# Performance work log

Measured on AMD Instinct MI355X. Metric: run time of the kernel, lower is better.

## Reference

```python
import jax, jax.numpy as jnp
import numpy as np

WINDOW_SIZE = (8, 8, 8)
DIM = 256
NUM_HEADS = 8
NUM_WINDOWS = 16
BATCH = 128  # num_windows * B
N = int(np.prod(WINDOW_SIZE))  # 512


def _make_rpb_buffers(ws):
    space = len(ws)
    coords = [np.arange(-(w - 1), w, dtype=np.float32) for w in ws]
    rpb = np.stack(np.meshgrid(*coords, indexing='ij'))  # (space, 2w-1, ...)
    for i in range(space):
        rpb[i] = rpb[i] / (ws[i] - 1)
    rpb = np.moveaxis(rpb, 0, -1)[None]  # (1, ..., space)
    rpb = 8.0 * rpb
    rpb = np.sign(rpb) * np.log2(np.abs(rpb) + 1.0) / np.log2(8.0)
    grid = np.stack(np.meshgrid(*[np.arange(w) for w in ws], indexing='ij'))
    g = grid.reshape(space, -1).astype(np.int64)
    dists = g[:, :, None] - g[:, None, :]  # (space, N, N)
    for i in range(space):
        center = max(int(np.prod([2 * w - 1 for w in ws[i + 1:]])), 1)
        dists[i] = (dists[i] + ws[i] - 1) * center
    rpb_idx = dists.sum(0)  # (N, N)
    return rpb.astype(np.float32), rpb_idx.astype(np.int32)


def setup_inputs() -> dict:
    key = jax.random.key(0)
    ks = jax.random.split(key, 8)
    rpb_np, rpb_idx_np = _make_rpb_buffers(WINDOW_SIZE)
    s = 0.02
    return {
        'x': jax.random.normal(ks[0], (BATCH, N, DIM), dtype=jnp.float32),
        'mask': jnp.zeros((NUM_WINDOWS, N, N), dtype=jnp.float32),
        'qkv_w': jax.random.normal(ks[1], (3 * DIM, DIM), dtype=jnp.float32) * s,
        'proj_w': jax.random.normal(ks[2], (DIM, DIM), dtype=jnp.float32) * s,
        'proj_b': jnp.zeros((DIM,), dtype=jnp.float32),
        'cpb_w1': jax.random.normal(ks[3], (512, 3), dtype=jnp.float32) * s,
        'cpb_b1': jnp.zeros((512,), dtype=jnp.float32),
        'cpb_w2': jax.random.normal(ks[4], (NUM_HEADS, 512), dtype=jnp.float32) * s,
        'rpb': jnp.asarray(rpb_np),
        'rpb_idx': jnp.asarray(rpb_idx_np),
    }


def reference(x, mask, qkv_w, proj_w, proj_b, cpb_w1, cpb_b1, cpb_w2, rpb, rpb_idx):
    b, n, c = x.shape
    h = cpb_w2.shape[0]
    hd = c // h
    # qkv projection (no bias), split into q,k,v of shape (b, h, n, hd)
    qkv = jnp.einsum('bnc,oc->bno', x, qkv_w).reshape(b, n, 3, h, hd)
    qkv = jnp.transpose(qkv, (2, 0, 3, 1, 4))
    q, k, v = qkv[0], qkv[1], qkv[2]
    # continuous relative-position bias: MLP over log-spaced coords, gather, sigmoid
    hidden = jax.nn.relu(jnp.einsum('...d,od->...o', rpb, cpb_w1) + cpb_b1)
    table = jnp.einsum('...o,ho->...h', hidden, cpb_w2).reshape(-1, h)  # (prod(2w-1), h)
    rpb_bias = table[rpb_idx.reshape(-1)].reshape(n, n, h)
    rpb_bias = 16.0 * jax.nn.sigmoid(rpb_bias)
    rpb_bias = jnp.transpose(rpb_bias, (2, 0, 1))[None]  # (1, h, n, n)
    # mask (nw, n, n) -> (b, 1, n, n) via repeat along batch
    nw = mask.shape[0]
    m = jnp.tile(mask[:, None, :, :], (b // nw, 1, 1, 1))
    bias = m + rpb_bias  # (b, h, n, n)
    # scaled dot-product attention
    scale = 1.0 / jnp.sqrt(jnp.float32(hd))
    scores = jnp.einsum('bhqd,bhkd->bhqk', q, k) * scale + bias
    attn = jax.nn.softmax(scores, axis=-1)
    out = jnp.einsum('bhqk,bhkd->bhqd', attn, v)
    out = jnp.transpose(out, (0, 2, 1, 3)).reshape(b, n, c)
    out = jnp.einsum('bnc,oc->bno', out, proj_w) + proj_b
    return out
```

## Files before the change

### kernel.cpp

```cpp
#include <hip/hip_runtime.h>
#include <hip/hip_bf16.h>


using u16 = unsigned short;
using u32 = unsigned int;
typedef short bf16x4 __attribute__((ext_vector_type(4)));
typedef short bf16x8 __attribute__((ext_vector_type(8)));
typedef float f32x4 __attribute__((ext_vector_type(4)));

#define QSL 0.25503471f
#define LOG2E 1.44269504f
#define CMB_SHIFT 11.65f

static __device__ __forceinline__ u32 cvt_pk_bf16(float lo, float hi) {
  u32 r;
  asm("v_cvt_pk_bf16_f32 %0, %1, %2" : "=v"(r) : "v"(lo), "v"(hi));
  return r;
}

__global__ __launch_bounds__(512) void cpb_kernel(
    const float* __restrict__ rpb, const float* __restrict__ w1,
    const float* __restrict__ b1, const float* __restrict__ w2,
    float* __restrict__ table16) {
  __shared__ float hid[512];
  const int p = blockIdx.x;
  const int t = threadIdx.x;
  const float r0 = rpb[p * 3 + 0], r1 = rpb[p * 3 + 1], r2 = rpb[p * 3 + 2];
  float hv = fmaf(r0, w1[t * 3 + 0],
             fmaf(r1, w1[t * 3 + 1],
             fmaf(r2, w1[t * 3 + 2], b1[t])));
  hid[t] = fmaxf(hv, 0.0f);
  __syncthreads();
  const int h = t >> 6, lane = t & 63;
  float s = 0.0f;
#pragma unroll
  for (int u = 0; u < 8; ++u)
    s = fmaf(hid[lane + u * 64], w2[h * 512 + lane + u * 64], s);
#pragma unroll
  for (int off = 32; off > 0; off >>= 1) s += __shfl_down(s, off);
  if (lane == 0) table16[p * 8 + h] = 23.08312065f / (1.0f + __expf(-s));
}

__global__ __launch_bounds__(256) void cmb_kernel(
    const int* __restrict__ rpb_idx, const float* __restrict__ table16,
    const float* __restrict__ mask, u16* __restrict__ cmb) {
  const int ij0 = (blockIdx.x * 256 + threadIdx.x) * 4;
  const int w = blockIdx.y;
  const float4 m4 = *reinterpret_cast<const float4*>(mask + (size_t)w * 262144 + ij0);
  const int4 i4 = *reinterpret_cast<const int4*>(rpb_idx + ij0);
  float ta[8], tb[8], tc[8], td[8];
  *reinterpret_cast<float4*>(&ta[0]) = *reinterpret_cast<const float4*>(table16 + i4.x * 8);
  *reinterpret_cast<float4*>(&ta[4]) = *reinterpret_cast<const float4*>(table16 + i4.x * 8 + 4);
  *reinterpret_cast<float4*>(&tb[0]) = *reinterpret_cast<const float4*>(table16 + i4.y * 8);
  *reinterpret_cast<float4*>(&tb[4]) = *reinterpret_cast<const float4*>(table16 + i4.y * 8 + 4);
  *reinterpret_cast<float4*>(&tc[0]) = *reinterpret_cast<const float4*>(table16 + i4.z * 8);
  *reinterpret_cast<float4*>(&tc[4]) = *reinterpret_cast<const float4*>(table16 + i4.z * 8 + 4);
  *reinterpret_cast<float4*>(&td[0]) = *reinterpret_cast<const float4*>(table16 + i4.w * 8);
  *reinterpret_cast<float4*>(&td[4]) = *reinterpret_cast<const float4*>(table16 + i4.w * 8 + 4);
  const float b0 = m4.x * LOG2E - CMB_SHIFT;
  const float b1 = m4.y * LOG2E - CMB_SHIFT;
  const float b2 = m4.z * LOG2E - CMB_SHIFT;
  const float b3 = m4.w * LOG2E - CMB_SHIFT;
  u16* outp = cmb + (size_t)w * 8 * 262144 + ij0;
#pragma unroll
  for (int h = 0; h < 8; ++h) {
    uint2 o;
    o.x = cvt_pk_bf16(ta[h] + b0, tb[h] + b1);
    o.y = cvt_pk_bf16(tc[h] + b2, td[h] + b3);
    *reinterpret_cast<uint2*>(outp + (size_t)h * 262144) = o;
  }
}

__global__ __launch_bounds__(256) void qkv_mfma(
    const float* __restrict__ x, const float* __restrict__ w,
    u16* __restrict__ qbuf, u16* __restrict__ kbuf, u16* __restrict__ vbuf) {
  __shared__ u16 As[128 * 64];
  __shared__ u16 Bs[128 * 64];
  const int tid = threadIdx.x;
  const int flat = blockIdx.x;
  const int wrk = (flat & 7) * 384 + (flat >> 3);
  const int bm = wrk / 6;
  const int bn = wrk - bm * 6;
  const int m0 = bm * 128, n0 = bn * 128;
  const float scl = (bn < 2) ? QSL : 1.0f;
  const int lane = tid & 63, wid = tid >> 6;
  const int wm = wid >> 1, wn = wid & 1;
  const int lq = lane & 15, g = lane >> 4;
  const f32x4 fz = {0.f, 0.f, 0.f, 0.f};
  f32x4 acc[4][4];
#pragma unroll
  for (int i = 0; i < 4; ++i)
#pragma unroll
    for (int j = 0; j < 4; ++j) acc[i][j] = fz;

  const int r0 = tid >> 3;
  const int ch = tid & 7;
  const int sx = (ch ^ (r0 & 7)) << 3;

  float4 ga[4][2], gb[4][2];
  auto gload = [&](int k0) {
#pragma unroll
    for (int rr = 0; rr < 4; ++rr) {
      const int r = r0 + rr * 32;
      const float* ax = x + (size_t)(m0 + r) * 256 + k0 + ch * 8;
      ga[rr][0] = *reinterpret_cast<const float4*>(ax);
      ga[rr][1] = *reinterpret_cast<const float4*>(ax + 4);
      const float* bx = w + (size_t)(n0 + r) * 256 + k0 + ch * 8;
      gb[rr][0] = *reinterpret_cast<const float4*>(bx);
      gb[rr][1] = *reinterpret_cast<const float4*>(bx + 4);
    }
  };

  gload(0);
  for (int k0 = 0; k0 < 256; k0 += 64) {
    __syncthreads();
#pragma unroll
    for (int rr = 0; rr < 4; ++rr) {
      const int r = r0 + rr * 32;
      uint4 pk;
      pk.x = cvt_pk_bf16(ga[rr][0].x, ga[rr][0].y);
      pk.y = cvt_pk_bf16(ga[rr][0].z, ga[rr][0].w);
      pk.z = cvt_pk_bf16(ga[rr][1].x, ga[rr][1].y);
      pk.w = cvt_pk_bf16(ga[rr][1].z, ga[rr][1].w);
      *reinterpret_cast<uint4*>(&As[r * 64 + sx]) = pk;
      pk.x = cvt_pk_bf16(gb[rr][0].x * scl, gb[rr][0].y * scl);
      pk.y = cvt_pk_bf16(gb[rr][0].z * scl, gb[rr][0].w * scl);
      pk.z = cvt_pk_bf16(gb[rr][1].x * scl, gb[rr][1].y * scl);
      pk.w = cvt_pk_bf16(gb[rr][1].z * scl, gb[rr][1].w * scl);
      *reinterpret_cast<uint4*>(&Bs[r * 64 + sx]) = pk;
    }
    __syncthreads();
    if (k0 + 64 < 256) gload(k0 + 64);
#pragma unroll
    for (int ks = 0; ks < 2; ++ks) {
      bf16x8 xf[4], wf[4];
#pragma unroll
      for (int mt = 0; mt < 4; ++mt) {
        const int row = wm * 64 + mt * 16 + lq;
        xf[mt] = *reinterpret_cast<const bf16x8*>(
            &As[row * 64 + (((ks * 4 + g) ^ (row & 7)) << 3)]);
      }
#pragma unroll
      for (int nt = 0; nt < 4; ++nt) {
        const int row = wn * 64 + nt * 16 + lq;
        wf[nt] = *reinterpret_cast<const bf16x8*>(
            &Bs[row * 64 + (((ks * 4 + g) ^ (row & 7)) << 3)]);
      }
#pragma unroll
      for (int mt = 0; mt < 4; ++mt)
#pragma unroll
        for (int nt = 0; nt < 4; ++nt)
          acc[mt][nt] = __builtin_amdgcn_mfma_f32_16x16x32_bf16(
              wf[nt], xf[mt], acc[mt][nt], 0, 0, 0);
    }
  }
  const int sec = bn >> 1;
  u16* dst = sec == 0 ? qbuf : (sec == 1 ? kbuf : vbuf);
#pragma unroll
  for (int mt = 0; mt < 4; ++mt) {
    const int m = m0 + wm * 64 + mt * 16 + lq;
    const int b = m >> 9, ii = m & 511;
#pragma unroll
    for (int nt = 0; nt < 4; ++nt) {
      const int n = n0 + wn * 64 + nt * 16 + 4 * g;
      const int h = (n & 255) >> 5;
      const int d = n & 31;
      const size_t off = ((size_t)(b * 8 + h) * 512 + ii) * 32 + d;
      uint2 o2;
      o2.x = cvt_pk_bf16(acc[mt][nt][0], acc[mt][nt][1]);
      o2.y = cvt_pk_bf16(acc[mt][nt][2], acc[mt][nt][3]);
      *reinterpret_cast<uint2*>(dst + off) = o2;
    }
  }
}

__global__ __launch_bounds__(256, 2) void attn_mfma(
    u16* qbuf,
    const u16* __restrict__ kbuf, const u16* __restrict__ vbuf,
    const u16* __restrict__ cmb) {
  __shared__ u16 Klds[512 * 32];
  __shared__ u16 Vtlds[32 * 512];
  const int t = threadIdx.x;
  const int qc = blockIdx.x, h = blockIdx.y;
  const int bz = blockIdx.z;
  const int b = ((bz & 15) << 3) | (bz >> 4);
  const size_t bh = (size_t)b * 8 + h;
  const u16* kb = kbuf + bh * 16384;
  const u16* vb = vbuf + bh * 16384;

#pragma unroll
  for (int c = 0; c < 8; ++c) {
    const int cid = t + c * 256;
    const int key = cid >> 2, ch = cid & 3;
    const uint4 kd = *reinterpret_cast<const uint4*>(kb + cid * 8);
    const int idx = key * 32 + ((ch * 8) ^ (((key >> 1) & 3) << 3));
    *reinterpret_cast<uint4*>(&Klds[idx]) = kd;
  }
#pragma unroll
  for (int r = 0; r < 2; ++r) {
    const int n = t + r * 256;
    const uint4 v0 = *reinterpret_cast<const uint4*>(vb + n * 32);
    const uint4 v1 = *reinterpret_cast<const uint4*>(vb + n * 32 + 8);
    const uint4 v2 = *reinterpret_cast<const uint4*>(vb + n * 32 + 16);
    const uint4 v3 = *reinterpret_cast<const uint4*>(vb + n * 32 + 24);
    const u32 wv16[16] = {v0.x, v0.y, v0.z, v0.w, v1.x, v1.y, v1.z, v1.w,
                          v2.x, v2.y, v2.z, v2.w, v3.x, v3.y, v3.z, v3.w};
#pragma unroll
    for (int u = 0; u < 16; ++u) {
      const int d0 = 2 * u, d1 = 2 * u + 1;
      Vtlds[d0 * 512 + (n ^ ((d0 & 7) << 3))] = (u16)(wv16[u] & 0xffffu);
      Vtlds[d1 * 512 + (n ^ ((d1 & 7) << 3))] = (u16)(wv16[u] >> 16);
    }
  }
  __syncthreads();

  const int lane = t & 63;
  const int lq = lane & 15, g = lane >> 4;
  const int wv = t >> 6;
  const int q0 = qc * 256 + wv * 64;

  bf16x8 Qf[4];
  u16* qrowbase = qbuf + bh * 16384;
#pragma unroll
  for (int qt = 0; qt < 4; ++qt)
    Qf[qt] = *reinterpret_cast<const bf16x8*>(qrowbase + (q0 + qt * 16 + lq) * 32 + g * 8);

  const u16* cmbp[4];
  const size_t whbase = (size_t)((b & 15) * 8 + h) * 262144;
#pragma unroll
  for (int qt = 0; qt < 4; ++qt)
    cmbp[qt] = cmb + whbase + (size_t)(q0 + qt * 16 + lq) * 512 + 4 * g;

  const f32x4 fzero = {0.f, 0.f, 0.f, 0.f};
  f32x4 o[2][4];
  f32x4 lsum4[4];
#pragma unroll
  for (int qt = 0; qt < 4; ++qt) {
    lsum4[qt] = fzero;
    o[0][qt] = fzero;
    o[1][qt] = fzero;
  }

  for (int j0 = 0; j0 < 512; j0 += 64) {
    bf16x8 Ak[4];
#pragma unroll
    for (int kt = 0; kt < 4; ++kt) {
      const int key = j0 + kt * 16 + lq;
      const int idx = key * 32 + ((g * 8) ^ (((key >> 1) & 3) << 3));
      Ak[kt] = *reinterpret_cast<const bf16x8*>(&Klds[idx]);
    }
    f32x4 s[4][4];
#pragma unroll
    for (int kt = 0; kt < 4; ++kt)
#pragma unroll
      for (int qt = 0; qt < 4; ++qt) {
        const uint2 cc = *reinterpret_cast<const uint2*>(cmbp[qt] + j0 + kt * 16);
        f32x4 ci;
        ci[0] = __uint_as_float((cc.x & 0xffffu) << 16);
        ci[1] = __uint_as_float(cc.x & 0xffff0000u);
        ci[2] = __uint_as_float((cc.y & 0xffffu) << 16);
        ci[3] = __uint_as_float(cc.y & 0xffff0000u);
        s[kt][qt] = __builtin_amdgcn_mfma_f32_16x16x32_bf16(Ak[kt], Qf[qt], ci, 0, 0, 0);
      }
#pragma unroll
    for (int kt = 0; kt < 4; ++kt) {
      bf16x4 Av[2];
#pragma unroll
      for (int dt = 0; dt < 2; ++dt) {
        const int d = dt * 16 + lq;
        const int n0 = j0 + kt * 16 + 4 * g;
        const int idx = d * 512 + (n0 ^ ((d & 7) << 3));
        Av[dt] = *reinterpret_cast<const bf16x4*>(&Vtlds[idx]);
      }
#pragma unroll
      for (int qt = 0; qt < 4; ++qt) {
        f32x4 p = s[kt][qt];
        p[0] = __builtin_amdgcn_exp2f(p[0]);
        p[1] = __builtin_amdgcn_exp2f(p[1]);
        p[2] = __builtin_amdgcn_exp2f(p[2]);
        p[3] = __builtin_amdgcn_exp2f(p[3]);
        lsum4[qt] += p;
        union { u32 u[2]; bf16x4 v; } bp;
        bp.u[0] = cvt_pk_bf16(p[0], p[1]);
        bp.u[1] = cvt_pk_bf16(p[2], p[3]);
        o[0][qt] = __builtin_amdgcn_mfma_f32_16x16x16bf16_1k(Av[0], bp.v, o[0][qt], 0, 0, 0);
        o[1][qt] = __builtin_amdgcn_mfma_f32_16x16x16bf16_1k(Av[1], bp.v, o[1][qt], 0, 0, 0);
      }
    }
  }
#pragma unroll
  for (int qt = 0; qt < 4; ++qt) {
    float l = (lsum4[qt][0] + lsum4[qt][1]) + (lsum4[qt][2] + lsum4[qt][3]);
    l += __shfl_xor(l, 16);
    l += __shfl_xor(l, 32);
    const float inv = 1.0f / l;
    u16* orow = qrowbase + (q0 + qt * 16 + lq) * 32;
#pragma unroll
    for (int dt = 0; dt < 2; ++dt) {
      uint2 w2;
      w2.x = cvt_pk_bf16(o[dt][qt][0] * inv, o[dt][qt][1] * inv);
      w2.y = cvt_pk_bf16(o[dt][qt][2] * inv, o[dt][qt][3] * inv);
      *reinterpret_cast<uint2*>(orow + dt * 16 + 4 * g) = w2;
    }
  }
}

__global__ __launch_bounds__(256, 2) void proj_mfma(
    const u16* __restrict__ abuf, const float* __restrict__ w,
    const float* __restrict__ pb, float* __restrict__ out) {
  __shared__ u16 As[128 * 64];
  __shared__ u16 Bs0[128 * 64];
  __shared__ u16 Bs1[128 * 64];
  const int tid = threadIdx.x;
  const int bm = blockIdx.x;
  const int m0 = bm * 128;
  const int lane = tid & 63, wid = tid >> 6;
  const int wm = wid >> 1, wn = wid & 1;
  const int lq = lane & 15, g = lane >> 4;
  const f32x4 fz = {0.f, 0.f, 0.f, 0.f};
  f32x4 acc0[4][4], acc1[4][4];
#pragma unroll
  for (int i = 0; i < 4; ++i)
#pragma unroll
    for (int j = 0; j < 4; ++j) { acc0[i][j] = fz; acc1[i][j] = fz; }

  const int r0 = tid >> 3;
  const int ch = tid & 7;
  const int sx = (ch ^ (r0 & 7)) << 3;
  const int ab = m0 >> 9;
  const u16* abase = abuf + (size_t)ab * 8 * 16384;
  const int dA0 = (ch & 3) * 8;

  for (int k0 = 0; k0 < 256; k0 += 64) {
    const int hA0 = (k0 >> 5) + (ch >> 2);
    __syncthreads();
#pragma unroll
    for (int rr = 0; rr < 4; ++rr) {
      const int r = r0 + rr * 32;
      const uint4 ga = *reinterpret_cast<const uint4*>(
          abase + ((size_t)hA0 * 512 + ((m0 & 511) + r)) * 32 + dA0);
      const float* bx0 = w + (size_t)r * 256 + k0 + ch * 8;
      const float* bx1 = w + (size_t)(128 + r) * 256 + k0 + ch * 8;
      const float4 b00 = *reinterpret_cast<const float4*>(bx0);
      const float4 b01 = *reinterpret_cast<const float4*>(bx0 + 4);
      const float4 b10 = *reinterpret_cast<const float4*>(bx1);
      const float4 b11 = *reinterpret_cast<const float4*>(bx1 + 4);
      *reinterpret_cast<uint4*>(&As[r * 64 + sx]) = ga;
      uint4 pk;
      pk.x = cvt_pk_bf16(b00.x, b00.y); pk.y = cvt_pk_bf16(b00.z, b00.w);
      pk.z = cvt_pk_bf16(b01.x, b01.y); pk.w = cvt_pk_bf16(b01.z, b01.w);
      *reinterpret_cast<uint4*>(&Bs0[r * 64 + sx]) = pk;
      pk.x = cvt_pk_bf16(b10.x, b10.y); pk.y = cvt_pk_bf16(b10.z, b10.w);
      pk.z = cvt_pk_bf16(b11.x, b11.y); pk.w = cvt_pk_bf16(b11.z, b11.w);
      *reinterpret_cast<uint4*>(&Bs1[r * 64 + sx]) = pk;
    }
    __syncthreads();
#pragma unroll
    for (int ks = 0; ks < 2; ++ks) {
      bf16x8 xf[4];
#pragma unroll
      for (int mt = 0; mt < 4; ++mt) {
        const int row = wm * 64 + mt * 16 + lq;
        xf[mt] = *reinterpret_cast<const bf16x8*>(
            &As[row * 64 + (((ks * 4 + g) ^ (row & 7)) << 3)]);
      }
#pragma unroll
      for (int nt = 0; nt < 4; ++nt) {
        const int row = wn * 64 + nt * 16 + lq;
        const int off = row * 64 + (((ks * 4 + g) ^ (row & 7)) << 3);
        const bf16x8 wf0 = *reinterpret_cast<const bf16x8*>(&Bs0[off]);
        const bf16x8 wf1 = *reinterpret_cast<const bf16x8*>(&Bs1[off]);
#pragma unroll
        for (int mt = 0; mt < 4; ++mt) {
          acc0[mt][nt] = __builtin_amdgcn_mfma_f32_16x16x32_bf16(
              wf0, xf[mt], acc0[mt][nt], 0, 0, 0);
          acc1[mt][nt] = __builtin_amdgcn_mfma_f32_16x16x32_bf16(
              wf1, xf[mt], acc1[mt][nt], 0, 0, 0);
        }
      }
    }
  }
#pragma unroll
  for (int mt = 0; mt < 4; ++mt) {
    const int m = m0 + wm * 64 + mt * 16 + lq;
#pragma unroll
    for (int nt = 0; nt < 4; ++nt) {
      const int n = wn * 64 + nt * 16 + 4 * g;
      const float4 pb0 = *reinterpret_cast<const float4*>(pb + n);
      *reinterpret_cast<float4*>(out + (size_t)m * 256 + n) =
          make_float4(acc0[mt][nt][0] + pb0.x, acc0[mt][nt][1] + pb0.y,
                      acc0[mt][nt][2] + pb0.z, acc0[mt][nt][3] + pb0.w);
      const float4 pb1 = *reinterpret_cast<const float4*>(pb + 128 + n);
      *reinterpret_cast<float4*>(out + (size_t)m * 256 + 128 + n) =
          make_float4(acc1[mt][nt][0] + pb1.x, acc1[mt][nt][1] + pb1.y,
                      acc1[mt][nt][2] + pb1.z, acc1[mt][nt][3] + pb1.w);
    }
  }
}

extern "C" void kernel_launch(void* const* d_in, const int* in_sizes, int n_in,
                              void* d_out, int out_size, void* d_ws, size_t ws_size,
                              hipStream_t stream) {
  const float* x = (const float*)d_in[0];
  const float* mask = (const float*)d_in[1];
  const float* qkv_w = (const float*)d_in[2];
  const float* proj_w = (const float*)d_in[3];
  const float* proj_b = (const float*)d_in[4];
  const float* cpb_w1 = (const float*)d_in[5];
  const float* cpb_b1 = (const float*)d_in[6];
  const float* cpb_w2 = (const float*)d_in[7];
  const float* rpb = (const float*)d_in[8];
  const int* rpb_idx = (const int*)d_in[9];
  float* out = (float*)d_out;

  char* ws = (char*)d_ws;
  u16* qbuf = (u16*)(ws);
  u16* kbuf = (u16*)(ws + 33554432);
  u16* vbuf = (u16*)(ws + 67108864);
  u16* cmb = (u16*)(ws + 100663296);
  float* table16 = (float*)(ws + 167772160);

  cpb_kernel<<<3375, 512, 0, stream>>>(rpb, cpb_w1, cpb_b1, cpb_w2, table16);
  cmb_kernel<<<dim3(256, 16), 256, 0, stream>>>(rpb_idx, table16, mask, cmb);
  qkv_mfma<<<3072, 256, 0, stream>>>(x, qkv_w, qbuf, kbuf, vbuf);
  attn_mfma<<<dim3(2, 8, 128), 256, 0, stream>>>(qbuf, kbuf, vbuf, cmb);
  proj_mfma<<<512, 256, 0, stream>>>(qbuf, proj_w, proj_b, out);
}
```

Baseline: 275.6 us.

## Widen QKV GEMM tile to 128x256 and drop register prefetch

The QKV projection kernel now computes a 128x256 output tile per block (two B tiles sharing one A tile), which halves the grid and halves the number of times the fp32 x tile is loaded and converted. The register-level prefetch of the next K slice is removed, so global loads are issued directly before the LDS store inside the loop. Accumulators double, so register pressure rises; launch bounds request 2 blocks per CU. The loss of load/compute overlap may offset the reuse gain.

```diff
diff --git a/kernel.cpp b/kernel.cpp
--- a/kernel.cpp
+++ b/kernel.cpp
@@ -71,69 +71,67 @@
   }
 }
 
-__global__ __launch_bounds__(256) void qkv_mfma(
+__global__ __launch_bounds__(256, 2) void qkv_mfma(
     const float* __restrict__ x, const float* __restrict__ w,
     u16* __restrict__ qbuf, u16* __restrict__ kbuf, u16* __restrict__ vbuf) {
   __shared__ u16 As[128 * 64];
-  __shared__ u16 Bs[128 * 64];
+  __shared__ u16 Bs0[128 * 64];
+  __shared__ u16 Bs1[128 * 64];
   const int tid = threadIdx.x;
   const int flat = blockIdx.x;
-  const int wrk = (flat & 7) * 384 + (flat >> 3);
-  const int bm = wrk / 6;
-  const int bn = wrk - bm * 6;
-  const int m0 = bm * 128, n0 = bn * 128;
-  const float scl = (bn < 2) ? QSL : 1.0f;
+  const int wrk = (flat & 7) * 192 + (flat >> 3);
+  const int bm = wrk / 3;
+  const int bnp = wrk - bm * 3;
+  const int m0 = bm * 128, n0 = bnp * 256;
+  const float scl = (bnp == 0) ? QSL : 1.0f;
+  u16* dst = bnp == 0 ? qbuf : (bnp == 1 ? kbuf : vbuf);
   const int lane = tid & 63, wid = tid >> 6;
   const int wm = wid >> 1, wn = wid & 1;
   const int lq = lane & 15, g = lane >> 4;
   const f32x4 fz = {0.f, 0.f, 0.f, 0.f};
-  f32x4 acc[4][4];
+  f32x4 acc0[4][4], acc1[4][4];
 #pragma unroll
   for (int i = 0; i < 4; ++i)
 #pragma unroll
-    for (int j = 0; j < 4; ++j) acc[i][j] = fz;
+    for (int j = 0; j < 4; ++j) { acc0[i][j] = fz; acc1[i][j] = fz; }
 
   const int r0 = tid >> 3;
   const int ch = tid & 7;
   const int sx = (ch ^ (r0 & 7)) << 3;
 
-  float4 ga[4][2], gb[4][2];
-  auto gload = [&](int k0) {
+  for (int k0 = 0; k0 < 256; k0 += 64) {
+    __syncthreads();
 #pragma unroll
     for (int rr = 0; rr < 4; ++rr) {
       const int r = r0 + rr * 32;
       const float* ax = x + (size_t)(m0 + r) * 256 + k0 + ch * 8;
-      ga[rr][0] = *reinterpret_cast<const float4*>(ax);
-      ga[rr][1] = *reinterpret_cast<const float4*>(ax + 4);
-      const float* bx = w + (size_t)(n0 + r) * 256 + k0 + ch * 8;
-      gb[rr][0] = *reinterpret_cast<const float4*>(bx);
-      gb[rr][1] = *reinterpret_cast<const float4*>(bx + 4);
-    }
-  };
-
-  gload(0);
-  for (int k0 = 0; k0 < 256; k0 += 64) {
+      const float4 a0 = *reinterpret_cast<const float4*>(ax);
+      const float4 a1 = *reinterpret_cast<const float4*>(ax + 4);
+      const float* bx0 = w + (size_t)(n0 + r) * 256 + k0 + ch * 8;
+      const float* bx1 = w + (size_t)(n0 + 128 + r) * 256 + k0 + ch * 8;
+      const float4 b00 = *reinterpret_cast<const float4*>(bx0);
+      const float4 b01 = *reinterpret_cast<const float4*>(bx0 + 4);
+      const float4 b10 = *reinterpret_cast<const float4*>(bx1);
+      const float4 b11 = *reinterpret_cast<const float4*>(bx1 + 4);
+      uint4 pk;
+      pk.x = cvt_pk_bf16(a0.x, a0.y); pk.y = cvt_pk_bf16(a0.z, a0.w);
+      pk.z = cvt_pk_bf16(a1.x, a1.y); pk.w = cvt_pk_bf16(a1.z, a1.w);
+      *reinterpret_cast<uint4*>(&As[r * 64 + sx]) = pk;
+      pk.x = cvt_pk_bf16(b00.x * scl, b00.y * scl);
+      pk.y = cvt_pk_bf16(b00.z * scl, b00.w * scl);
+      pk.z = cvt_pk_bf16(b01.x * scl, b01.y * scl);
+      pk.w = cvt_pk_bf16(b01.z * scl, b01.w * scl);
+      *reinterpret_cast<uint4*>(&Bs0[r * 64 + sx]) = pk;
+      pk.x = cvt_pk_bf16(b10.x * scl, b10.y * scl);
+      pk.y = cvt_pk_bf16(b10.z * scl, b10.w * scl);
+      pk.z = cvt_pk_bf16(b11.x * scl, b11.y * scl);
+      pk.w = cvt_pk_bf16(b11.z * scl, b11.w * scl);
+      *reinterpret_cast<uint4*>(&Bs1[r * 64 + sx]) = pk;
+    }
     __syncthreads();
 #pragma unroll
-    for (int rr = 0; rr < 4; ++rr) {
-      const int r = r0 + rr * 32;
-      uint4 pk;
-      pk.x = cvt_pk_bf16(ga[rr][0].x, ga[rr][0].y);
-      pk.y = cvt_pk_bf16(ga[rr][0].z, ga[rr][0].w);
-      pk.z = cvt_pk_bf16(ga[rr][1].x, ga[rr][1].y);
-      pk.w = cvt_pk_bf16(ga[rr][1].z, ga[rr][1].w);
-      *reinterpret_cast<uint4*>(&As[r * 64 + sx]) = pk;
-      pk.x = cvt_pk_bf16(gb[rr][0].x * scl, gb[rr][0].y * scl);
-      pk.y = cvt_pk_bf16(gb[rr][0].z * scl, gb[rr][0].w * scl);
-      pk.z = cvt_pk_bf16(gb[rr][1].x * scl, gb[rr][1].y * scl);
-      pk.w = cvt_pk_bf16(gb[rr][1].z * scl, gb[rr][1].w * scl);
-      *reinterpret_cast<uint4*>(&Bs[r * 64 + sx]) = pk;
-    }
-    __syncthreads();
-    if (k0 + 64 < 256) gload(k0 + 64);
-#pragma unroll
     for (int ks = 0; ks < 2; ++ks) {
-      bf16x8 xf[4], wf[4];
+      bf16x8 xf[4];
 #pragma unroll
       for (int mt = 0; mt < 4; ++mt) {
         const int row = wm * 64 + mt * 16 + lq;
@@ -143,33 +141,46 @@
 #pragma unroll
       for (int nt = 0; nt < 4; ++nt) {
         const int row = wn * 64 + nt * 16 + lq;
-        wf[nt] = *reinterpret_cast<const bf16x8*>(
-            &Bs[row * 64 + (((ks * 4 + g) ^ (row & 7)) << 3)]);
-      }
-#pragma unroll
-      for (int mt = 0; mt < 4; ++mt)
-#pragma unroll
-        for (int nt = 0; nt < 4; ++nt)
-          acc[mt][nt] = __builtin_amdgcn_mfma_f32_16x16x32_bf16(
-              wf[nt], xf[mt], acc[mt][nt], 0, 0, 0);
-    }
-  }
-  const int sec = bn >> 1;
-  u16* dst = sec == 0 ? qbuf : (sec == 1 ? kbuf : vbuf);
+        const int off = row * 64 + (((ks * 4 + g) ^ (row & 7)) << 3);
+        const bf16x8 wf0 = *reinterpret_cast<const bf16x8*>(&Bs0[off]);
+        const bf16x8 wf1 = *reinterpret_cast<const bf16x8*>(&Bs1[off]);
+#pragma unroll
+        for (int mt = 0; mt < 4; ++mt) {
+          acc0[mt][nt] = __builtin_amdgcn_mfma_f32_16x16x32_bf16(
+              wf0, xf[mt], acc0[mt][nt], 0, 0, 0);
+          acc1[mt][nt] = __builtin_amdgcn_mfma_f32_16x16x32_bf16(
+              wf1, xf[mt], acc1[mt][nt], 0, 0, 0);
+        }
+      }
+    }
+  }
 #pragma unroll
   for (int mt = 0; mt < 4; ++mt) {
     const int m = m0 + wm * 64 + mt * 16 + lq;
     const int b = m >> 9, ii = m & 511;
 #pragma unroll
     for (int nt = 0; nt < 4; ++nt) {
-      const int n = n0 + wn * 64 + nt * 16 + 4 * g;
-      const int h = (n & 255) >> 5;
-      const int d = n & 31;
-      const size_t off = ((size_t)(b * 8 + h) * 512 + ii) * 32 + d;
-      uint2 o2;
-      o2.x = cvt_pk_bf16(acc[mt][nt][0], acc[mt][nt][1]);
-      o2.y = cvt_pk_bf16(acc[mt][nt][2], acc[mt][nt][3]);
-      *reinterpret_cast<uint2*>(dst + off) = o2;
+      const int nn = wn * 64 + nt * 16 + 4 * g;
+      {
+        const int n = n0 + nn;
+        const int h = (n & 255) >> 5;
+        const int d = n & 31;
+        const size_t off = ((size_t)(b * 8 + h) * 512 + ii) * 32 + d;
+        uint2 o2;
+        o2.x = cvt_pk_bf16(acc0[mt][nt][0], acc0[mt][nt][1]);
+        o2.y = cvt_pk_bf16(acc0[mt][nt][2], acc0[mt][nt][3]);
+        *reinterpret_cast<uint2*>(dst + off) = o2;
+      }
+      {
+        const int n = n0 + 128 + nn;
+        const int h = (n & 255) >> 5;
+        const int d = n & 31;
+        const size_t off = ((size_t)(b * 8 + h) * 512 + ii) * 32 + d;
+        uint2 o2;
+        o2.x = cvt_pk_bf16(acc1[mt][nt][0], acc1[mt][nt][1]);
+        o2.y = cvt_pk_bf16(acc1[mt][nt][2], acc1[mt][nt][3]);
+        *reinterpret_cast<uint2*>(dst + off) = o2;
+      }
     }
   }
 }
@@ -422,7 +433,7 @@
 
   cpb_kernel<<<3375, 512, 0, stream>>>(rpb, cpb_w1, cpb_b1, cpb_w2, table16);
   cmb_kernel<<<dim3(256, 16), 256, 0, stream>>>(rpb_idx, table16, mask, cmb);
-  qkv_mfma<<<3072, 256, 0, stream>>>(x, qkv_w, qbuf, kbuf, vbuf);
+  qkv_mfma<<<1536, 256, 0, stream>>>(x, qkv_w, qbuf, kbuf, vbuf);
   attn_mfma<<<dim3(2, 8, 128), 256, 0, stream>>>(qbuf, kbuf, vbuf, cmb);
   proj_mfma<<<512, 256, 0, stream>>>(qbuf, proj_w, proj_b, out);
 }
```

Result: no change. 275.9 us (+0.1%).
